# Kernel optimization log

Hardware: AMD Instinct MI355X
Metric: run time of the kernel (lower is better)

The kernel has to match this reference:

```python
import jax, jax.numpy as jnp
import numpy as np

NEG_SLOPE = 0.2
EPS = 1e-16


def setup_inputs() -> dict:
    N, E, IN, H, C = 100000, 1600000, 128, 4, 16
    key = jax.random.key(0)
    k1, k2, k3, k4, k5 = jax.random.split(key, 5)
    x = jax.random.normal(k1, (N, IN), dtype=jnp.float32)
    edge_index = jax.random.randint(k2, (2, E), 0, N, dtype=jnp.int64)
    # Xavier-uniform init like nn.init.xavier_uniform_
    limW = float(np.sqrt(6.0 / (IN + H * C)))
    W = jax.random.uniform(k3, (IN, H * C), dtype=jnp.float32, minval=-limW, maxval=limW)
    lima = float(np.sqrt(6.0 / (H + C)))
    att = jax.random.uniform(k4, (1, H, C), dtype=jnp.float32, minval=-lima, maxval=lima)
    bias = jnp.zeros((H * C,), dtype=jnp.float32)
    return {"x": x, "edge_index": edge_index, "W": W, "att": att, "bias": bias}


def reference(x, edge_index, W, att, bias):
    N = x.shape[0]
    H, C = att.shape[1], att.shape[2]
    h = (x @ W).reshape(N, H, C)  # [N,H,C]
    # add self loops
    loops = jnp.arange(N, dtype=edge_index.dtype)
    row = jnp.concatenate([edge_index[0], loops])  # target nodes
    col = jnp.concatenate([edge_index[1], loops])  # source nodes
    x_i = h[row]  # [Etot,H,C]
    x_j = h[col]
    e = jax.nn.leaky_relu(x_i + x_j, NEG_SLOPE)
    alpha = jnp.einsum('ehc,hc->eh', e, att[0])  # [Etot,H]
    # segment softmax keyed by row (every node has a self loop -> no empty segments)
    amax = jax.lax.stop_gradient(jax.ops.segment_max(alpha, row, num_segments=N))
    ea = jnp.exp(alpha - amax[row])
    denom = jax.ops.segment_sum(ea, row, num_segments=N)
    alpha = ea / (denom[row] + EPS)
    # weighted message scatter-add (dropout p=0 / eval mode)
    out = jax.ops.segment_sum(x_j * alpha[:, :, None], row, num_segments=N)  # [N,H,C]
    out = out.reshape(N, H * C) + bias  # concat=True
    return out
```

## Files before the change

kernel.cpp:

```cpp
#include <hip/hip_runtime.h>

#define NEG_SLOPE 0.2f

typedef float f32x2 __attribute__((ext_vector_type(2)));
typedef float f32x4 __attribute__((ext_vector_type(4)));
typedef short bf16x8 __attribute__((ext_vector_type(8)));

__device__ __forceinline__ unsigned short f2bf(float f) {
  union { float f; unsigned u; } v; v.f = f;
  unsigned r = v.u + 0x7fff + ((v.u >> 16) & 1);
  return (unsigned short)(r >> 16);
}
__device__ __forceinline__ float bf2f(unsigned short u) {
  union { unsigned u; float f; } v; v.u = ((unsigned)u) << 16;
  return v.f;
}
__device__ __forceinline__ unsigned pkbf(float a, float b) {
  return (unsigned)f2bf(a) | ((unsigned)f2bf(b) << 16);
}
__device__ __forceinline__ f32x4 upk4(uint2 u) {
  union { unsigned u; float f; } a, b, c, d;
  a.u = u.x << 16; b.u = u.x & 0xffff0000u;
  c.u = u.y << 16; d.u = u.y & 0xffff0000u;
  f32x4 r; r.x = a.f; r.y = b.f; r.z = c.f; r.w = d.f;
  return r;
}

__global__ __launch_bounds__(256) void gemm_mfma(const float* __restrict__ x,
                                                 const float* __restrict__ W,
                                                 unsigned short* __restrict__ hb, int N) {
  __shared__ uint4 Bl[1024];
  const int t = threadIdx.x;
  {
    const int l = t & 63;
    const int kt = (t >> 6) & 3;
    const int kb = kt * 32 + ((l >> 4) * 8);
    const int cb = l & 15;
#pragma unroll
    for (int ct = 0; ct < 4; ct++) {
      const float* wp = W + (size_t)kb * 64 + ct * 16 + cb;
      unsigned p[4];
#pragma unroll
      for (int jj = 0; jj < 4; jj++)
        p[jj] = pkbf(wp[(2 * jj) * 64], wp[(2 * jj + 1) * 64]);
      Bl[(ct * 4 + kt) * 64 + l] = make_uint4(p[0], p[1], p[2], p[3]);
    }
  }
  __syncthreads();
  const int l = t & 63;
  const int wv = t >> 6;
  union BU { bf16x8 v; uint4 q; };
  BU b[4][4];
#pragma unroll
  for (int ct = 0; ct < 4; ct++)
#pragma unroll
    for (int kt = 0; kt < 4; kt++) b[ct][kt].q = Bl[(ct * 4 + kt) * 64 + l];

  const int rowbase0 = blockIdx.x * 256 + wv * 64;
#pragma unroll
  for (int rt = 0; rt < 4; rt++) {
    const int rbase = rowbase0 + rt * 16;
    int rl = rbase + (l & 15);
    if (rl >= N) rl = N - 1;
    const float* xp = x + (size_t)rl * 128 + ((l >> 4) * 8);
    BU ah[4], alo[4];
#pragma unroll
    for (int kt = 0; kt < 4; kt++) {
      float f[8];
      float4 v0 = *(const float4*)(xp + kt * 32);
      float4 v1 = *(const float4*)(xp + kt * 32 + 4);
      f[0] = v0.x; f[1] = v0.y; f[2] = v0.z; f[3] = v0.w;
      f[4] = v1.x; f[5] = v1.y; f[6] = v1.z; f[7] = v1.w;
      unsigned short hs[8], ls[8];
#pragma unroll
      for (int j = 0; j < 8; j++) {
        hs[j] = f2bf(f[j]);
        ls[j] = f2bf(f[j] - bf2f(hs[j]));
      }
      ah[kt].q = make_uint4(hs[0] | (hs[1] << 16), hs[2] | (hs[3] << 16),
                            hs[4] | (hs[5] << 16), hs[6] | (hs[7] << 16));
      alo[kt].q = make_uint4(ls[0] | (ls[1] << 16), ls[2] | (ls[3] << 16),
                             ls[4] | (ls[5] << 16), ls[6] | (ls[7] << 16));
    }
#pragma unroll
    for (int ct = 0; ct < 4; ct++) {
      f32x4 acc = {0.f, 0.f, 0.f, 0.f};
#pragma unroll
      for (int kt = 0; kt < 4; kt++) {
        acc = __builtin_amdgcn_mfma_f32_16x16x32_bf16(ah[kt].v, b[ct][kt].v, acc, 0, 0, 0);
        acc = __builtin_amdgcn_mfma_f32_16x16x32_bf16(alo[kt].v, b[ct][kt].v, acc, 0, 0, 0);
      }
#pragma unroll
      for (int j = 0; j < 4; j++) {
        float v = acc[j];
        float pv = __shfl_xor(v, 1);
        int row = rbase + (l >> 4) * 4 + j;
        if (!(l & 1) && row < N) {
          *(unsigned*)((char*)hb + (size_t)row * 128 + ct * 32 + (l & 15) * 2) =
              pkbf(v, pv);
        }
      }
    }
  }
}

#define TILE 2048
#define NBKT_MAX 256

__global__ __launch_bounds__(256) void bucket_pass(const int* __restrict__ rowi,
                                                   const int* __restrict__ coli,
                                                   int* __restrict__ bucket_fill,
                                                   unsigned* __restrict__ bucket_arr,
                                                   int E, int C, int NBKT) {
  __shared__ int cnt[NBKT_MAX];
  __shared__ int base[NBKT_MAX];
  const int t = threadIdx.x;
  const int tile0 = blockIdx.x * TILE;
  for (int i = t; i < NBKT_MAX; i += 256) cnt[i] = 0;
  __syncthreads();
  unsigned pk[8];
  int bk[8];
#pragma unroll
  for (int j = 0; j < 8; j++) {
    int i = tile0 + j * 256 + t;
    if (i < E) {
      int r = rowi[i];
      int c = coli[i];
      bk[j] = r >> 9;
      pk[j] = ((unsigned)(r & 511) << 17) | (unsigned)c;
      atomicAdd(&cnt[bk[j]], 1);
    } else {
      bk[j] = -1;
    }
  }
  __syncthreads();
  if (t < NBKT) {
    int n = cnt[t];
    base[t] = (n > 0) ? atomicAdd(&bucket_fill[t], n) : 0;
    cnt[t] = 0;
  }
  __syncthreads();
#pragma unroll
  for (int j = 0; j < 8; j++) {
    if (bk[j] >= 0) {
      int lp = atomicAdd(&cnt[bk[j]], 1);
      int pos = base[bk[j]] + lp;
      if (pos < C) bucket_arr[bk[j] * C + pos] = pk[j];
    }
  }
}

#define STAGE_CAP 10240

__global__ __launch_bounds__(256) void csr_pass(unsigned* __restrict__ bucket_arr,
                                                const int* __restrict__ bucket_fill,
                                                int* __restrict__ offs,
                                                int* __restrict__ rowend,
                                                int C, int N) {
  __shared__ unsigned stage[STAGE_CAP];
  __shared__ int hist[512], excl[512], pairs[256];
  const int t = threadIdx.x;
  const int b = blockIdx.x;
  const int bb = b * C;
  const int nb = min(bucket_fill[b], C);
  for (int i = t; i < 512; i += 256) hist[i] = 0;
  for (int i = t; i < nb; i += 256) stage[i] = bucket_arr[bb + i];
  __syncthreads();
  for (int i = t; i < nb; i += 256) atomicAdd(&hist[stage[i] >> 17], 1);
  __syncthreads();
  int h0 = hist[2 * t], h1 = hist[2 * t + 1];
  int ps = h0 + h1;
  pairs[t] = ps;
  __syncthreads();
  for (int off = 1; off < 256; off <<= 1) {
    int val = pairs[t] + ((t >= off) ? pairs[t - off] : 0);
    __syncthreads();
    pairs[t] = val;
    __syncthreads();
  }
  int pexcl = pairs[t] - ps;
  excl[2 * t] = pexcl;
  excl[2 * t + 1] = pexcl + h0;
  __syncthreads();
  const int r0 = b << 9;
  for (int r = t; r < 512; r += 256) {
    int gr = r0 + r;
    if (gr < N) {
      int o = bb + excl[r];
      offs[gr] = o;
      rowend[gr] = o + hist[r];
    }
  }
  __syncthreads();
  for (int i = t; i < nb; i += 256) {
    unsigned pk = stage[i];
    int r = pk >> 17;
    int lp = atomicAdd(&excl[r], 1);
    bucket_arr[bb + lp] = (pk & 0x1FFFFu) << 7;
  }
}

#define ESTEP(u)                                        \
  {                                                     \
    f32x4 jv = upk4(u);                                 \
    f32x4 s = hiv + jv;                                 \
    f32x4 as;                                           \
    as.x = fabsf(s.x); as.y = fabsf(s.y);               \
    as.z = fabsf(s.z); as.w = fabsf(s.w);               \
    f32x4 d = s * attA + as * attB;                     \
    float al = (d.x + d.y) + (d.z + d.w);               \
    al += __shfl_xor(al, 1);                            \
    al += __shfl_xor(al, 2);                            \
    float p = __expf(al);                               \
    acc += jv * p;                                      \
    den += p;                                           \
  }

__global__ __launch_bounds__(256) void node_pass(const unsigned short* __restrict__ hb,
                                                 const int* __restrict__ offs,
                                                 const int* __restrict__ rowend,
                                                 const unsigned* __restrict__ srcs,
                                                 const float* __restrict__ att,
                                                 const float* __restrict__ bias,
                                                 float* __restrict__ out, int N) {
  int w = (blockIdx.x * blockDim.x + threadIdx.x) >> 6;
  if (w >= N) return;
  const int lane = threadIdx.x & 63;
  const int lr = lane & 15;
  const int q = lane >> 4;
  const char* hbc = (const char*)hb;
  const unsigned loff = (unsigned)(lr << 3);
  const f32x4 attv = *(const f32x4*)(att + 4 * lr);
  const f32x4 attA = attv * 0.6f;
  const f32x4 attB = attv * 0.4f;
  const f32x4 hiv = upk4(*(const uint2*)(hbc + (((unsigned)w << 7) | loff)));
  f32x4 acc;
  float den;
  {
    f32x4 s = hiv + hiv;
    f32x4 as;
    as.x = fabsf(s.x); as.y = fabsf(s.y);
    as.z = fabsf(s.z); as.w = fabsf(s.w);
    f32x4 d = s * attA + as * attB;
    float al = (d.x + d.y) + (d.z + d.w);
    al += __shfl_xor(al, 1);
    al += __shfl_xor(al, 2);
    float p = (q == 0) ? __expf(al) : 0.f;
    acc = hiv * p;
    den = p;
  }
  int k = offs[w];
  const int k1 = rowend[w];
  for (; k + 8 <= k1; k += 8) {
    unsigned o0 = srcs[k + q] | loff;
    unsigned o1 = srcs[k + 4 + q] | loff;
    uint2 u0 = *(const uint2*)(hbc + o0);
    uint2 u1 = *(const uint2*)(hbc + o1);
    ESTEP(u0);
    ESTEP(u1);
  }
  for (; k < k1; k += 4) {
    int kk = k + q;
    bool act = kk < k1;
    unsigned o = (act ? srcs[kk] : ((unsigned)w << 7)) | loff;
    uint2 u = *(const uint2*)(hbc + o);
    f32x4 jv = upk4(u);
    f32x4 s = hiv + jv;
    f32x4 as;
    as.x = fabsf(s.x); as.y = fabsf(s.y);
    as.z = fabsf(s.z); as.w = fabsf(s.w);
    f32x4 d = s * attA + as * attB;
    float al = (d.x + d.y) + (d.z + d.w);
    al += __shfl_xor(al, 1);
    al += __shfl_xor(al, 2);
    float p = act ? __expf(al) : 0.f;
    acc += jv * p;
    den += p;
  }
  acc.x += __shfl_xor(acc.x, 16); acc.y += __shfl_xor(acc.y, 16);
  acc.z += __shfl_xor(acc.z, 16); acc.w += __shfl_xor(acc.w, 16);
  den += __shfl_xor(den, 16);
  acc.x += __shfl_xor(acc.x, 32); acc.y += __shfl_xor(acc.y, 32);
  acc.z += __shfl_xor(acc.z, 32); acc.w += __shfl_xor(acc.w, 32);
  den += __shfl_xor(den, 32);
  if (q == 0) {
    float inv = 1.0f / (den + 1e-16f);
    f32x4 bv = *(const f32x4*)(bias + 4 * lr);
    f32x4 o = acc * inv + bv;
    *(f32x4*)(out + (size_t)w * 64 + 4 * lr) = o;
  }
}

extern "C" void kernel_launch(void* const* d_in, const int* in_sizes, int n_in,
                              void* d_out, int out_size, void* d_ws, size_t ws_size,
                              hipStream_t stream) {
  const float* x = (const float*)d_in[0];
  const int* eidx = (const int*)d_in[1];
  const float* W = (const float*)d_in[2];
  const float* att = (const float*)d_in[3];
  const float* bias = (const float*)d_in[4];
  float* out = (float*)d_out;

  const int N = in_sizes[0] / 128;
  const int E = in_sizes[1] / 2;
  const int NBKT = (N + 511) >> 9;
  int C = (E + NBKT - 1) / NBKT;
  C = C + C / 8 + 64;
  C = (C + 15) & ~15;
  if (C > STAGE_CAP) C = STAGE_CAP;

  unsigned short* hb = (unsigned short*)d_ws;
  int* bucket_fill = (int*)(hb + (size_t)N * 64);
  int* offs = bucket_fill + NBKT_MAX;
  int* rowend = offs + N;
  unsigned* bucket_arr = (unsigned*)(rowend + N);

  hipMemsetAsync(bucket_fill, 0, NBKT_MAX * sizeof(int), stream);

  gemm_mfma<<<(N + 255) / 256, 256, 0, stream>>>(x, W, hb, N);
  bucket_pass<<<(E + TILE - 1) / TILE, 256, 0, stream>>>(eidx, eidx + E, bucket_fill,
                                                         bucket_arr, E, C, NBKT);
  csr_pass<<<NBKT, 256, 0, stream>>>(bucket_arr, bucket_fill, offs, rowend, C, N);
  node_pass<<<(N * 64 + 255) / 256, 256, 0, stream>>>(hb, offs, rowend, bucket_arr, att,
                                                      bias, out, N);
}
```

Before: 120.3 us.

## Insert self loops into CSR, pack row ranges, widen edge and gather unrolls

```diff
diff --git a/kernel.cpp b/kernel.cpp
--- a/kernel.cpp
+++ b/kernel.cpp
@@ -104,24 +104,25 @@
   }
 }
 
-#define TILE 2048
+#define TILE 4096
+#define EPT 16
 #define NBKT_MAX 256
 
 __global__ __launch_bounds__(256) void bucket_pass(const int* __restrict__ rowi,
                                                    const int* __restrict__ coli,
                                                    int* __restrict__ bucket_fill,
                                                    unsigned* __restrict__ bucket_arr,
-                                                   int E, int C, int NBKT) {
+                                                   int E, int Cedge, int Ctot, int NBKT) {
   __shared__ int cnt[NBKT_MAX];
   __shared__ int base[NBKT_MAX];
   const int t = threadIdx.x;
   const int tile0 = blockIdx.x * TILE;
   for (int i = t; i < NBKT_MAX; i += 256) cnt[i] = 0;
   __syncthreads();
-  unsigned pk[8];
-  int bk[8];
-#pragma unroll
-  for (int j = 0; j < 8; j++) {
+  unsigned pk[EPT];
+  int bk[EPT];
+#pragma unroll
+  for (int j = 0; j < EPT; j++) {
     int i = tile0 + j * 256 + t;
     if (i < E) {
       int r = rowi[i];
@@ -141,11 +142,11 @@
   }
   __syncthreads();
 #pragma unroll
-  for (int j = 0; j < 8; j++) {
+  for (int j = 0; j < EPT; j++) {
     if (bk[j] >= 0) {
       int lp = atomicAdd(&cnt[bk[j]], 1);
       int pos = base[bk[j]] + lp;
-      if (pos < C) bucket_arr[bk[j] * C + pos] = pk[j];
+      if (pos < Cedge) bucket_arr[bk[j] * Ctot + pos] = pk[j];
     }
   }
 }
@@ -154,16 +155,16 @@
 
 __global__ __launch_bounds__(256) void csr_pass(unsigned* __restrict__ bucket_arr,
                                                 const int* __restrict__ bucket_fill,
-                                                int* __restrict__ offs,
-                                                int* __restrict__ rowend,
-                                                int C, int N) {
+                                                int2* __restrict__ rowinfo,
+                                                int Cedge, int Ctot, int N) {
   __shared__ unsigned stage[STAGE_CAP];
   __shared__ int hist[512], excl[512], pairs[256];
   const int t = threadIdx.x;
   const int b = blockIdx.x;
-  const int bb = b * C;
-  const int nb = min(bucket_fill[b], C);
-  for (int i = t; i < 512; i += 256) hist[i] = 0;
+  const int bb = b * Ctot;
+  const int r0 = b << 9;
+  const int nb = min(bucket_fill[b], Cedge);
+  for (int i = t; i < 512; i += 256) hist[i] = ((r0 + i) < N) ? 1 : 0;
   for (int i = t; i < nb; i += 256) stage[i] = bucket_arr[bb + i];
   __syncthreads();
   for (int i = t; i < nb; i += 256) atomicAdd(&hist[stage[i] >> 17], 1);
@@ -182,13 +183,11 @@
   excl[2 * t] = pexcl;
   excl[2 * t + 1] = pexcl + h0;
   __syncthreads();
-  const int r0 = b << 9;
   for (int r = t; r < 512; r += 256) {
     int gr = r0 + r;
     if (gr < N) {
       int o = bb + excl[r];
-      offs[gr] = o;
-      rowend[gr] = o + hist[r];
+      rowinfo[gr] = make_int2(o, o + hist[r]);
     }
   }
   __syncthreads();
@@ -197,6 +196,11 @@
     int r = pk >> 17;
     int lp = atomicAdd(&excl[r], 1);
     bucket_arr[bb + lp] = (pk & 0x1FFFFu) << 7;
+  }
+  __syncthreads();
+  for (int r = t; r < 512; r += 256) {
+    int gr = r0 + r;
+    if (gr < N) bucket_arr[bb + excl[r]] = (unsigned)gr << 7;
   }
 }
 
@@ -217,8 +221,7 @@
   }
 
 __global__ __launch_bounds__(256) void node_pass(const unsigned short* __restrict__ hb,
-                                                 const int* __restrict__ offs,
-                                                 const int* __restrict__ rowend,
+                                                 const int2* __restrict__ rowinfo,
                                                  const unsigned* __restrict__ srcs,
                                                  const float* __restrict__ att,
                                                  const float* __restrict__ bias,
@@ -233,36 +236,35 @@
   const f32x4 attv = *(const f32x4*)(att + 4 * lr);
   const f32x4 attA = attv * 0.6f;
   const f32x4 attB = attv * 0.4f;
+  const int2 oi = rowinfo[w];
+  int k = oi.x;
+  const int k1 = oi.y;
   const f32x4 hiv = upk4(*(const uint2*)(hbc + (((unsigned)w << 7) | loff)));
-  f32x4 acc;
-  float den;
-  {
-    f32x4 s = hiv + hiv;
-    f32x4 as;
-    as.x = fabsf(s.x); as.y = fabsf(s.y);
-    as.z = fabsf(s.z); as.w = fabsf(s.w);
-    f32x4 d = s * attA + as * attB;
-    float al = (d.x + d.y) + (d.z + d.w);
-    al += __shfl_xor(al, 1);
-    al += __shfl_xor(al, 2);
-    float p = (q == 0) ? __expf(al) : 0.f;
-    acc = hiv * p;
-    den = p;
-  }
-  int k = offs[w];
-  const int k1 = rowend[w];
-  for (; k + 8 <= k1; k += 8) {
+  f32x4 acc = {0.f, 0.f, 0.f, 0.f};
+  float den = 0.f;
+  for (; k + 16 <= k1; k += 16) {
     unsigned o0 = srcs[k + q] | loff;
     unsigned o1 = srcs[k + 4 + q] | loff;
+    unsigned o2 = srcs[k + 8 + q] | loff;
+    unsigned o3 = srcs[k + 12 + q] | loff;
     uint2 u0 = *(const uint2*)(hbc + o0);
     uint2 u1 = *(const uint2*)(hbc + o1);
+    uint2 u2 = *(const uint2*)(hbc + o2);
+    uint2 u3 = *(const uint2*)(hbc + o3);
     ESTEP(u0);
     ESTEP(u1);
-  }
-  for (; k < k1; k += 4) {
+    ESTEP(u2);
+    ESTEP(u3);
+  }
+  for (; k + 4 <= k1; k += 4) {
+    unsigned o = srcs[k + q] | loff;
+    uint2 u = *(const uint2*)(hbc + o);
+    ESTEP(u);
+  }
+  if (k < k1) {
     int kk = k + q;
     bool act = kk < k1;
-    unsigned o = (act ? srcs[kk] : ((unsigned)w << 7)) | loff;
+    unsigned o = (act ? srcs[kk] : srcs[k]) | loff;
     uint2 u = *(const uint2*)(hbc + o);
     f32x4 jv = upk4(u);
     f32x4 s = hiv + jv;
@@ -304,23 +306,23 @@
   const int N = in_sizes[0] / 128;
   const int E = in_sizes[1] / 2;
   const int NBKT = (N + 511) >> 9;
-  int C = (E + NBKT - 1) / NBKT;
-  C = C + C / 8 + 64;
-  C = (C + 15) & ~15;
-  if (C > STAGE_CAP) C = STAGE_CAP;
+  int Cedge = (E + NBKT - 1) / NBKT;
+  Cedge = Cedge + Cedge / 8 + 64;
+  Cedge = (Cedge + 15) & ~15;
+  if (Cedge > STAGE_CAP) Cedge = STAGE_CAP;
+  const int Ctot = Cedge + 512;
 
   unsigned short* hb = (unsigned short*)d_ws;
   int* bucket_fill = (int*)(hb + (size_t)N * 64);
-  int* offs = bucket_fill + NBKT_MAX;
-  int* rowend = offs + N;
-  unsigned* bucket_arr = (unsigned*)(rowend + N);
+  int2* rowinfo = (int2*)(bucket_fill + NBKT_MAX);
+  unsigned* bucket_arr = (unsigned*)(rowinfo + N);
 
   hipMemsetAsync(bucket_fill, 0, NBKT_MAX * sizeof(int), stream);
 
   gemm_mfma<<<(N + 255) / 256, 256, 0, stream>>>(x, W, hb, N);
   bucket_pass<<<(E + TILE - 1) / TILE, 256, 0, stream>>>(eidx, eidx + E, bucket_fill,
-                                                         bucket_arr, E, C, NBKT);
-  csr_pass<<<NBKT, 256, 0, stream>>>(bucket_arr, bucket_fill, offs, rowend, C, N);
-  node_pass<<<(N * 64 + 255) / 256, 256, 0, stream>>>(hb, offs, rowend, bucket_arr, att,
-                                                      bias, out, N);
-}
+                                                         bucket_arr, E, Cedge, Ctot, NBKT);
+  csr_pass<<<NBKT, 256, 0, stream>>>(bucket_arr, bucket_fill, rowinfo, Cedge, Ctot, N);
+  node_pass<<<(N * 64 + 255) / 256, 256, 0, stream>>>(hb, rowinfo, bucket_arr, att, bias,
+                                                      out, N);
+}
```

Result: faster. 115.7 us (-3.9%).
